# Optimization experiments

Measured on AMD Instinct MI355X. Metric: run time of the kernel, lower is better.

## Reference

```python
import jax, jax.numpy as jnp
import numpy as np

D_MODEL = 1024
NUM_HEADS = 16
D_HEAD = D_MODEL // NUM_HEADS


def setup_inputs() -> dict:
    key = jax.random.key(0)
    ks = jax.random.split(key, 11)
    B, S = 2, 2048
    s = 1.0 / np.sqrt(D_MODEL)
    inp = {
        "Q": jax.random.normal(ks[0], (B, S, D_MODEL), dtype=jnp.float32),
        "K": jax.random.normal(ks[1], (B, S, D_MODEL), dtype=jnp.float32),
        "V": jax.random.normal(ks[2], (B, S, D_MODEL), dtype=jnp.float32),
        "W_q": jax.random.normal(ks[3], (D_MODEL, D_MODEL), dtype=jnp.float32) * s,
        "b_q": jnp.zeros((D_MODEL,), dtype=jnp.float32),
        "W_k": jax.random.normal(ks[4], (D_MODEL, D_MODEL), dtype=jnp.float32) * s,
        "b_k": jnp.zeros((D_MODEL,), dtype=jnp.float32),
        "W_v": jax.random.normal(ks[5], (D_MODEL, D_MODEL), dtype=jnp.float32) * s,
        "b_v": jnp.zeros((D_MODEL,), dtype=jnp.float32),
        "W_o": jax.random.normal(ks[6], (D_MODEL, D_MODEL), dtype=jnp.float32) * s,
        "b_o": jnp.zeros((D_MODEL,), dtype=jnp.float32),
    }
    return inp


def reference(Q, K, V, W_q, b_q, W_k, b_k, W_v, b_v, W_o, b_o):
    B, S, _ = Q.shape
    # Linear projections (torch Linear: x @ W.T + b)
    q = Q @ W_q.T + b_q  # [B,S,D]
    k = K @ W_k.T + b_k
    v = V @ W_v.T + b_v
    # split heads -> [B,H,S,d]
    q = q.reshape(B, S, NUM_HEADS, D_HEAD).transpose(0, 2, 1, 3)
    k = k.reshape(B, S, NUM_HEADS, D_HEAD).transpose(0, 2, 1, 3)
    v = v.reshape(B, S, NUM_HEADS, D_HEAD).transpose(0, 2, 1, 3)
    scores = jnp.einsum("bhqd,bhkd->bhqk", q, k) / np.sqrt(D_HEAD).astype(np.float32)
    attn = jax.nn.softmax(scores, axis=-1)
    out = jnp.einsum("bhqk,bhkd->bhqd", attn, v)
    out = out.transpose(0, 2, 1, 3).reshape(B, S, D_MODEL)
    return out @ W_o.T + b_o
```

## Files before the change

### kernel.cpp

```cpp
#include <hip/hip_runtime.h>
#include <stdint.h>

#define D_MODEL 1024
#define S_LEN   2048
#define BATCH   2
#define NHEAD   16
#define DHEAD   64
#define NTOK    (BATCH * S_LEN)

typedef unsigned short u16;
typedef __attribute__((ext_vector_type(8))) short bf16x8;
typedef __attribute__((ext_vector_type(4))) float f32x4;
typedef __attribute__((ext_vector_type(2))) unsigned int u32x2;

__device__ __forceinline__ unsigned pack2bf(float lo, float hi) {
    unsigned a = __float_as_uint(lo) + 0x8000u;
    unsigned b = __float_as_uint(hi) + 0x8000u;
    return __builtin_amdgcn_perm(b, a, 0x07060302u);
}
__device__ __forceinline__ u16 f2bf1(float f) {
    return (u16)((__float_as_uint(f) + 0x8000u) >> 16);
}

#define GAS(p) ((const __attribute__((address_space(1))) void*)(p))
#define LAS(p) ((__attribute__((address_space(3))) void*)(p))
#define SWZ8(row, c) (((((row) << 3) | ((c) ^ ((row) & 7)))) << 3)

__global__ __launch_bounds__(256) void convert_kernel(
    const float* __restrict__ Q, const float* __restrict__ K, const float* __restrict__ V,
    const float* __restrict__ Wq, const float* __restrict__ Wk,
    const float* __restrict__ Wv, const float* __restrict__ Wo,
    u16* __restrict__ Qb, u16* __restrict__ Kb, u16* __restrict__ Vb,
    u16* __restrict__ Wqb, u16* __restrict__ Wkb, u16* __restrict__ Wvb, u16* __restrict__ Wob)
{
    const size_t SEG = 262144;
    size_t start = (size_t)blockIdx.x * 4096;
    int s = (int)(start / SEG);
    const float* src; u16* dst; size_t seg0;
    if (s < 4)       { src = Q;  dst = Qb;  seg0 = 0; }
    else if (s < 8)  { src = K;  dst = Kb;  seg0 = 4 * SEG; }
    else if (s < 12) { src = V;  dst = Vb;  seg0 = 8 * SEG; }
    else if (s == 12){ src = Wq; dst = Wqb; seg0 = 12 * SEG; }
    else if (s == 13){ src = Wk; dst = Wkb; seg0 = 13 * SEG; }
    else if (s == 14){ src = Wv; dst = Wvb; seg0 = 14 * SEG; }
    else             { src = Wo; dst = Wob; seg0 = 15 * SEG; }
    size_t off = start - seg0 + threadIdx.x;
    const float4* s4 = (const float4*)src;
    #pragma unroll
    for (int k = 0; k < 16; ++k) {
        float4 x = s4[off + (size_t)k * 256];
        u32x2 p = (u32x2){pack2bf(x.x, x.y), pack2bf(x.z, x.w)};
        *(u32x2*)(dst + (off + (size_t)k * 256) * 4) = p;
    }
}

__global__ __launch_bounds__(256) void proj_kernel(
    const u16* __restrict__ Qb, const u16* __restrict__ Kb, const u16* __restrict__ Vb,
    const u16* __restrict__ Wqb, const u16* __restrict__ Wkb, const u16* __restrict__ Wvb,
    const float* __restrict__ bq, const float* __restrict__ bk, const float* __restrict__ bv,
    u16* __restrict__ qw, u16* __restrict__ kw, u16* __restrict__ vtw)
{
    const int z = blockIdx.z;
    const int bx = blockIdx.x;
    const u16* A    = (z == 0) ? Qb  : (z == 1) ? Kb  : Wvb;
    const u16* B    = (z == 0) ? Wqb : (z == 1) ? Wkb : Vb;
    const float* bias = (z == 0) ? bq : (z == 1) ? bk : bv;
    const int mbase = ((z == 2) ? (bx & 7) : (bx >> 3)) * 128;
    const int nbase = ((z == 2) ? (bx >> 3) : (bx & 7)) * 128;

    const int tid = threadIdx.x, lane = tid & 63, wave = tid >> 6;
    const int m16 = lane & 15, quad = lane >> 4;
    const int wm = wave >> 1, wn = wave & 1;

    __shared__ __align__(16) u16 As[128 * 64];
    __shared__ __align__(16) u16 Bs[128 * 64];

    int srow[4], scg[4];
    #pragma unroll
    for (int c = 0; c < 4; ++c) {
        int p = (wave * 4 + c) * 64 + lane;
        srow[c] = p >> 3;
        scg[c]  = (p & 7) ^ (srow[c] & 7);
    }

    f32x4 acc[4][4];
    #pragma unroll
    for (int mt = 0; mt < 4; ++mt)
        #pragma unroll
        for (int nt = 0; nt < 4; ++nt) acc[mt][nt] = (f32x4){0.f, 0.f, 0.f, 0.f};

    for (int kc = 0; kc < D_MODEL; kc += 64) {
        #pragma unroll
        for (int c = 0; c < 4; ++c) {
            __builtin_amdgcn_global_load_lds(
                GAS(A + (size_t)(mbase + srow[c]) * D_MODEL + kc + scg[c] * 8),
                LAS(As + (wave * 4 + c) * 512), 16, 0, 0);
            __builtin_amdgcn_global_load_lds(
                GAS(B + (size_t)(nbase + srow[c]) * D_MODEL + kc + scg[c] * 8),
                LAS(Bs + (wave * 4 + c) * 512), 16, 0, 0);
        }
        __syncthreads();
        #pragma unroll
        for (int half = 0; half < 2; ++half) {
            bf16x8 af[4], bfr[4];
            #pragma unroll
            for (int mt = 0; mt < 4; ++mt)
                af[mt] = *(const bf16x8*)&As[SWZ8(wm * 64 + mt * 16 + m16, quad + 4 * half)];
            #pragma unroll
            for (int nt = 0; nt < 4; ++nt)
                bfr[nt] = *(const bf16x8*)&Bs[SWZ8(wn * 64 + nt * 16 + m16, quad + 4 * half)];
            #pragma unroll
            for (int mt = 0; mt < 4; ++mt)
                #pragma unroll
                for (int nt = 0; nt < 4; ++nt)
                    acc[mt][nt] = __builtin_amdgcn_mfma_f32_16x16x32_bf16(af[mt], bfr[nt], acc[mt][nt], 0, 0, 0);
        }
        __syncthreads();
    }

    if (z < 2) {
        u16* dst = z ? kw : qw;
        const float scale = z ? 1.0f : 0.18033688011112042f;
        #pragma unroll
        for (int nt = 0; nt < 4; ++nt) {
            int gn = nbase + wn * 64 + nt * 16 + m16;
            float bb = bias[gn];
            #pragma unroll
            for (int mt = 0; mt < 4; ++mt)
                #pragma unroll
                for (int r = 0; r < 4; ++r) {
                    int gm = mbase + wm * 64 + mt * 16 + quad * 4 + r;
                    dst[(size_t)gm * D_MODEL + gn] = f2bf1((acc[mt][nt][r] + bb) * scale);
                }
        }
    } else {
        #pragma unroll
        for (int mt = 0; mt < 4; ++mt)
            #pragma unroll
            for (int r = 0; r < 4; ++r) {
                int gm = mbase + wm * 64 + mt * 16 + quad * 4 + r;
                float bb = bias[gm];
                #pragma unroll
                for (int nt = 0; nt < 4; ++nt) {
                    int gn = nbase + wn * 64 + nt * 16 + m16;
                    vtw[(size_t)gm * NTOK + gn] = f2bf1(acc[mt][nt][r] + bb);
                }
            }
    }
}

__global__ __launch_bounds__(256, 4) void attn_kernel(
    const u16* __restrict__ qw, const u16* __restrict__ kw,
    const u16* __restrict__ vtw, u16* __restrict__ aw)
{
    const int qbase = blockIdx.x * 128;
    const int h = blockIdx.y, b = blockIdx.z;
    const int tid = threadIdx.x, lane = tid & 63, wave = tid >> 6;
    const int m16 = lane & 15, quad = lane >> 4;
    const int colbase = h * DHEAD;
    const size_t qrow0 = (size_t)b * S_LEN + qbase;

    __shared__ __align__(16) u16 Ks[2][64 * 64];
    __shared__ __align__(16) u16 Vs[2][64 * 64];
    __shared__ __align__(16) u16 Ps[4][32][72];

    int srow[2], scg[2];
    #pragma unroll
    for (int i = 0; i < 2; ++i) {
        int p = (wave * 2 + i) * 64 + lane;
        srow[i] = p >> 3;
        scg[i]  = (p & 7) ^ (srow[i] & 7);
    }

    #define STAGE_KV(buf, kv0)                                                              \
        do {                                                                                \
            _Pragma("unroll")                                                               \
            for (int i_ = 0; i_ < 2; ++i_) {                                                \
                __builtin_amdgcn_global_load_lds(                                           \
                    GAS(kw + ((size_t)b * S_LEN + (kv0) + srow[i_]) * D_MODEL + colbase + scg[i_] * 8), \
                    LAS(Ks[buf] + (wave * 2 + i_) * 512), 16, 0, 0);                        \
                __builtin_amdgcn_global_load_lds(                                           \
                    GAS(vtw + (size_t)(colbase + srow[i_]) * NTOK + (size_t)b * S_LEN + (kv0) + scg[i_] * 8), \
                    LAS(Vs[buf] + (wave * 2 + i_) * 512), 16, 0, 0);                        \
            }                                                                               \
        } while (0)

    bf16x8 qf[2][2];
    #pragma unroll
    for (int mt = 0; mt < 2; ++mt)
        #pragma unroll
        for (int half = 0; half < 2; ++half)
            qf[mt][half] = *(const bf16x8*)(qw + (qrow0 + wave * 32 + mt * 16 + m16) * D_MODEL
                                            + colbase + quad * 8 + 32 * half);

    STAGE_KV(0, 0);

    float l[2][4];
    f32x4 o[2][4];
    #pragma unroll
    for (int mt = 0; mt < 2; ++mt) {
        #pragma unroll
        for (int r = 0; r < 4; ++r) l[mt][r] = 0.f;
        #pragma unroll
        for (int nt = 0; nt < 4; ++nt) o[mt][nt] = (f32x4){0.f, 0.f, 0.f, 0.f};
    }

    __syncthreads();

    for (int t = 0; t < S_LEN / 64; ++t) {
        const int cur = t & 1;
        if (t + 1 < S_LEN / 64) STAGE_KV(!cur, (t + 1) * 64);

        bf16x8 kf[4][2];
        #pragma unroll
        for (int nt = 0; nt < 4; ++nt)
            #pragma unroll
            for (int half = 0; half < 2; ++half)
                kf[nt][half] = *(const bf16x8*)&Ks[cur][SWZ8(nt * 16 + m16, quad + 4 * half)];

        f32x4 s[2][4];
        #pragma unroll
        for (int mt = 0; mt < 2; ++mt)
            #pragma unroll
            for (int nt = 0; nt < 4; ++nt) {
                s[mt][nt] = (f32x4){-12.f, -12.f, -12.f, -12.f};
                s[mt][nt] = __builtin_amdgcn_mfma_f32_16x16x32_bf16(qf[mt][0], kf[nt][0], s[mt][nt], 0, 0, 0);
                s[mt][nt] = __builtin_amdgcn_mfma_f32_16x16x32_bf16(qf[mt][1], kf[nt][1], s[mt][nt], 0, 0, 0);
            }

        bf16x8 vf[4][2];
        #pragma unroll
        for (int nt = 0; nt < 4; ++nt)
            #pragma unroll
            for (int half = 0; half < 2; ++half)
                vf[nt][half] = *(const bf16x8*)&Vs[cur][SWZ8(nt * 16 + m16, quad + 4 * half)];

        #pragma unroll
        for (int mt = 0; mt < 2; ++mt)
            #pragma unroll
            for (int r = 0; r < 4; ++r) {
                float p0 = __builtin_amdgcn_exp2f(s[mt][0][r]);
                float p1 = __builtin_amdgcn_exp2f(s[mt][1][r]);
                float p2 = __builtin_amdgcn_exp2f(s[mt][2][r]);
                float p3 = __builtin_amdgcn_exp2f(s[mt][3][r]);
                l[mt][r] += (p0 + p1) + (p2 + p3);
                int prow = mt * 16 + quad * 4 + r;
                Ps[wave][prow][0 * 16 + m16] = f2bf1(p0);
                Ps[wave][prow][1 * 16 + m16] = f2bf1(p1);
                Ps[wave][prow][2 * 16 + m16] = f2bf1(p2);
                Ps[wave][prow][3 * 16 + m16] = f2bf1(p3);
            }

        bf16x8 pf[2][2];
        #pragma unroll
        for (int mt = 0; mt < 2; ++mt)
            #pragma unroll
            for (int half = 0; half < 2; ++half)
                pf[mt][half] = *(const bf16x8*)&Ps[wave][mt * 16 + m16][half * 32 + quad * 8];

        #pragma unroll
        for (int mt = 0; mt < 2; ++mt)
            #pragma unroll
            for (int nt = 0; nt < 4; ++nt) {
                o[mt][nt] = __builtin_amdgcn_mfma_f32_16x16x32_bf16(pf[mt][0], vf[nt][0], o[mt][nt], 0, 0, 0);
                o[mt][nt] = __builtin_amdgcn_mfma_f32_16x16x32_bf16(pf[mt][1], vf[nt][1], o[mt][nt], 0, 0, 0);
            }

        __syncthreads();
    }

    #pragma unroll
    for (int mt = 0; mt < 2; ++mt)
        #pragma unroll
        for (int r = 0; r < 4; ++r) {
            float lv = l[mt][r];
            #pragma unroll
            for (int d = 1; d < 16; d <<= 1) lv += __shfl_xor(lv, d, 16);
            float inv = 1.0f / lv;
            size_t gm = qrow0 + wave * 32 + mt * 16 + quad * 4 + r;
            #pragma unroll
            for (int nt = 0; nt < 4; ++nt)
                aw[gm * D_MODEL + colbase + nt * 16 + m16] = f2bf1(o[mt][nt][r] * inv);
        }
    #undef STAGE_KV
}

__global__ __launch_bounds__(256) void outproj_kernel(
    const u16* __restrict__ aw, const u16* __restrict__ Wob,
    const float* __restrict__ bo, float* __restrict__ out)
{
    const int mbase = blockIdx.y * 64;
    const int nbase = blockIdx.x * 128;
    const int tid = threadIdx.x, lane = tid & 63, wave = tid >> 6;
    const int m16 = lane & 15, quad = lane >> 4;

    __shared__ __align__(16) u16 As[64 * 64];
    __shared__ __align__(16) u16 Bs[128 * 64];

    int arow[2], acg[2], brow[4], bcg[4];
    #pragma unroll
    for (int c = 0; c < 2; ++c) {
        int p = (wave * 2 + c) * 64 + lane;
        arow[c] = p >> 3; acg[c] = (p & 7) ^ (arow[c] & 7);
    }
    #pragma unroll
    for (int c = 0; c < 4; ++c) {
        int p = (wave * 4 + c) * 64 + lane;
        brow[c] = p >> 3; bcg[c] = (p & 7) ^ (brow[c] & 7);
    }

    f32x4 acc[4][2];
    #pragma unroll
    for (int mt = 0; mt < 4; ++mt)
        #pragma unroll
        for (int nt = 0; nt < 2; ++nt) acc[mt][nt] = (f32x4){0.f, 0.f, 0.f, 0.f};

    for (int kc = 0; kc < D_MODEL; kc += 64) {
        #pragma unroll
        for (int c = 0; c < 2; ++c)
            __builtin_amdgcn_global_load_lds(
                GAS(aw + (size_t)(mbase + arow[c]) * D_MODEL + kc + acg[c] * 8),
                LAS(As + (wave * 2 + c) * 512), 16, 0, 0);
        #pragma unroll
        for (int c = 0; c < 4; ++c)
            __builtin_amdgcn_global_load_lds(
                GAS(Wob + (size_t)(nbase + brow[c]) * D_MODEL + kc + bcg[c] * 8),
                LAS(Bs + (wave * 4 + c) * 512), 16, 0, 0);
        __syncthreads();
        #pragma unroll
        for (int half = 0; half < 2; ++half) {
            bf16x8 af[4], bfr[2];
            #pragma unroll
            for (int mt = 0; mt < 4; ++mt)
                af[mt] = *(const bf16x8*)&As[SWZ8(mt * 16 + m16, quad + 4 * half)];
            #pragma unroll
            for (int nt = 0; nt < 2; ++nt)
                bfr[nt] = *(const bf16x8*)&Bs[SWZ8(wave * 32 + nt * 16 + m16, quad + 4 * half)];
            #pragma unroll
            for (int mt = 0; mt < 4; ++mt)
                #pragma unroll
                for (int nt = 0; nt < 2; ++nt)
                    acc[mt][nt] = __builtin_amdgcn_mfma_f32_16x16x32_bf16(af[mt], bfr[nt], acc[mt][nt], 0, 0, 0);
        }
        __syncthreads();
    }

    #pragma unroll
    for (int nt = 0; nt < 2; ++nt) {
        int gn = nbase + wave * 32 + nt * 16 + m16;
        float bb = bo[gn];
        #pragma unroll
        for (int mt = 0; mt < 4; ++mt)
            #pragma unroll
            for (int r = 0; r < 4; ++r) {
                int gm = mbase + mt * 16 + quad * 4 + r;
                out[(size_t)gm * D_MODEL + gn] = acc[mt][nt][r] + bb;
            }
    }
}

extern "C" void kernel_launch(void* const* d_in, const int* in_sizes, int n_in,
                              void* d_out, int out_size, void* d_ws, size_t ws_size,
                              hipStream_t stream) {
    const float* Q  = (const float*)d_in[0];
    const float* K  = (const float*)d_in[1];
    const float* V  = (const float*)d_in[2];
    const float* Wq = (const float*)d_in[3];
    const float* bq = (const float*)d_in[4];
    const float* Wk = (const float*)d_in[5];
    const float* bk = (const float*)d_in[6];
    const float* Wv = (const float*)d_in[7];
    const float* bv = (const float*)d_in[8];
    const float* Wo = (const float*)d_in[9];
    const float* bo = (const float*)d_in[10];

    const size_t NT = (size_t)NTOK * D_MODEL;
    const size_t WN = (size_t)D_MODEL * D_MODEL;
    u16* base = (u16*)d_ws;
    u16* qw  = base;
    u16* kw  = base + NT;
    u16* vtw = base + 2 * NT;
    u16* Qb  = base + 3 * NT;
    u16* Kb  = base + 4 * NT;
    u16* Vb  = base + 5 * NT;
    u16* Wqb = base + 6 * NT;
    u16* Wkb = Wqb + WN;
    u16* Wvb = Wkb + WN;
    u16* Wob = Wvb + WN;
    u16* aww = Qb;

    convert_kernel<<<1024, 256, 0, stream>>>(Q, K, V, Wq, Wk, Wv, Wo,
                                             Qb, Kb, Vb, Wqb, Wkb, Wvb, Wob);
    proj_kernel<<<dim3(256, 1, 3), 256, 0, stream>>>(Qb, Kb, Vb, Wqb, Wkb, Wvb,
                                                     bq, bk, bv, qw, kw, vtw);
    attn_kernel<<<dim3(S_LEN / 128, NHEAD, BATCH), 256, 0, stream>>>(qw, kw, vtw, aww);
    outproj_kernel<<<dim3(D_MODEL / 128, NTOK / 64), 256, 0, stream>>>(
        aww, Wob, bo, (float*)d_out);
}
```

Before: 234.9 us.

## Transpose MFMA operand roles to vectorize epilogue stores and shrink attention query tiles

The Q/K projection and output projection now put the weights in the A operand and the tokens in the B operand, so each lane holds four consecutive output features. Those results are written with packed 8-byte bf16 stores or float4 stores instead of scalar 2-byte or 4-byte stores. Attention now computes S^T = K·Q^T with 16 query rows per wave and 64 per block, which doubles the grid. The P tile goes through a swizzled per-wave LDS buffer using packed writes. The aim is to cut uncoalesced stores and LDS traffic, at the cost of less K/V reuse per block, since each block now loads K/V for half as many queries.

```diff
diff --git a/kernel.cpp b/kernel.cpp
--- a/kernel.cpp
+++ b/kernel.cpp
@@ -62,11 +62,11 @@
 {
     const int z = blockIdx.z;
     const int bx = blockIdx.x;
-    const u16* A    = (z == 0) ? Qb  : (z == 1) ? Kb  : Wvb;
-    const u16* B    = (z == 0) ? Wqb : (z == 1) ? Wkb : Vb;
+    const u16* A = (z == 0) ? Wqb : (z == 1) ? Wkb : Wvb;
+    const u16* B = (z == 0) ? Qb  : (z == 1) ? Kb  : Vb;
     const float* bias = (z == 0) ? bq : (z == 1) ? bk : bv;
-    const int mbase = ((z == 2) ? (bx & 7) : (bx >> 3)) * 128;
-    const int nbase = ((z == 2) ? (bx >> 3) : (bx & 7)) * 128;
+    const int mbase = (bx & 7) * 128;
+    const int nbase = (bx >> 3) * 128;
 
     const int tid = threadIdx.x, lane = tid & 63, wave = tid >> 6;
     const int m16 = lane & 15, quad = lane >> 4;
@@ -119,31 +119,34 @@
     }
 
     if (z < 2) {
-        u16* dst = z ? kw : qw;
+        u16* Y = z ? kw : qw;
         const float scale = z ? 1.0f : 0.18033688011112042f;
         #pragma unroll
-        for (int nt = 0; nt < 4; ++nt) {
-            int gn = nbase + wn * 64 + nt * 16 + m16;
-            float bb = bias[gn];
-            #pragma unroll
-            for (int mt = 0; mt < 4; ++mt)
-                #pragma unroll
-                for (int r = 0; r < 4; ++r) {
-                    int gm = mbase + wm * 64 + mt * 16 + quad * 4 + r;
-                    dst[(size_t)gm * D_MODEL + gn] = f2bf1((acc[mt][nt][r] + bb) * scale);
-                }
+        for (int mt = 0; mt < 4; ++mt) {
+            int d0 = mbase + wm * 64 + mt * 16 + quad * 4;
+            float4 b4 = *(const float4*)&bias[d0];
+            #pragma unroll
+            for (int nt = 0; nt < 4; ++nt) {
+                int tok = nbase + wn * 64 + nt * 16 + m16;
+                float v0 = (acc[mt][nt][0] + b4.x) * scale;
+                float v1 = (acc[mt][nt][1] + b4.y) * scale;
+                float v2 = (acc[mt][nt][2] + b4.z) * scale;
+                float v3 = (acc[mt][nt][3] + b4.w) * scale;
+                *(u32x2*)(Y + (size_t)tok * D_MODEL + d0) =
+                    (u32x2){pack2bf(v0, v1), pack2bf(v2, v3)};
+            }
         }
     } else {
         #pragma unroll
         for (int mt = 0; mt < 4; ++mt)
             #pragma unroll
             for (int r = 0; r < 4; ++r) {
-                int gm = mbase + wm * 64 + mt * 16 + quad * 4 + r;
-                float bb = bias[gm];
+                int dout = mbase + wm * 64 + mt * 16 + quad * 4 + r;
+                float bb = bias[dout];
                 #pragma unroll
                 for (int nt = 0; nt < 4; ++nt) {
-                    int gn = nbase + wn * 64 + nt * 16 + m16;
-                    vtw[(size_t)gm * NTOK + gn] = f2bf1(acc[mt][nt][r] + bb);
+                    int tok = nbase + wn * 64 + nt * 16 + m16;
+                    vtw[(size_t)dout * NTOK + tok] = f2bf1(acc[mt][nt][r] + bb);
                 }
             }
     }
@@ -153,7 +156,7 @@
     const u16* __restrict__ qw, const u16* __restrict__ kw,
     const u16* __restrict__ vtw, u16* __restrict__ aw)
 {
-    const int qbase = blockIdx.x * 128;
+    const int qbase = blockIdx.x * 64;
     const int h = blockIdx.y, b = blockIdx.z;
     const int tid = threadIdx.x, lane = tid & 63, wave = tid >> 6;
     const int m16 = lane & 15, quad = lane >> 4;
@@ -162,7 +165,8 @@
 
     __shared__ __align__(16) u16 Ks[2][64 * 64];
     __shared__ __align__(16) u16 Vs[2][64 * 64];
-    __shared__ __align__(16) u16 Ps[4][32][72];
+    __shared__ __align__(16) u16 Pt[4][16 * 64];
+    u16* ptw = Pt[wave];
 
     int srow[2], scg[2];
     #pragma unroll
@@ -185,103 +189,80 @@
             }                                                                               \
         } while (0)
 
-    bf16x8 qf[2][2];
-    #pragma unroll
-    for (int mt = 0; mt < 2; ++mt)
-        #pragma unroll
-        for (int half = 0; half < 2; ++half)
-            qf[mt][half] = *(const bf16x8*)(qw + (qrow0 + wave * 32 + mt * 16 + m16) * D_MODEL
-                                            + colbase + quad * 8 + 32 * half);
+    bf16x8 qf[2];
+    #pragma unroll
+    for (int half = 0; half < 2; ++half)
+        qf[half] = *(const bf16x8*)(qw + (qrow0 + wave * 16 + m16) * D_MODEL
+                                    + colbase + half * 32 + quad * 8);
 
     STAGE_KV(0, 0);
 
-    float l[2][4];
-    f32x4 o[2][4];
-    #pragma unroll
-    for (int mt = 0; mt < 2; ++mt) {
-        #pragma unroll
-        for (int r = 0; r < 4; ++r) l[mt][r] = 0.f;
-        #pragma unroll
-        for (int nt = 0; nt < 4; ++nt) o[mt][nt] = (f32x4){0.f, 0.f, 0.f, 0.f};
-    }
-
+    float l = 0.f;
+    f32x4 o[4];
+    #pragma unroll
+    for (int nt = 0; nt < 4; ++nt) o[nt] = (f32x4){0.f, 0.f, 0.f, 0.f};
+
+    const int M = m16 & 7;
     __syncthreads();
 
     for (int t = 0; t < S_LEN / 64; ++t) {
         const int cur = t & 1;
         if (t + 1 < S_LEN / 64) STAGE_KV(!cur, (t + 1) * 64);
 
-        bf16x8 kf[4][2];
-        #pragma unroll
-        for (int nt = 0; nt < 4; ++nt)
+        f32x4 s[4];
+        #pragma unroll
+        for (int nt = 0; nt < 4; ++nt) {
+            bf16x8 kf0 = *(const bf16x8*)&Ks[cur][SWZ8(nt * 16 + m16, quad)];
+            bf16x8 kf1 = *(const bf16x8*)&Ks[cur][SWZ8(nt * 16 + m16, quad + 4)];
+            s[nt] = (f32x4){-12.f, -12.f, -12.f, -12.f};
+            s[nt] = __builtin_amdgcn_mfma_f32_16x16x32_bf16(kf0, qf[0], s[nt], 0, 0, 0);
+            s[nt] = __builtin_amdgcn_mfma_f32_16x16x32_bf16(kf1, qf[1], s[nt], 0, 0, 0);
+        }
+
+        bf16x8 vf[4][2];
+        #pragma unroll
+        for (int ntd = 0; ntd < 4; ++ntd)
             #pragma unroll
             for (int half = 0; half < 2; ++half)
-                kf[nt][half] = *(const bf16x8*)&Ks[cur][SWZ8(nt * 16 + m16, quad + 4 * half)];
-
-        f32x4 s[2][4];
-        #pragma unroll
-        for (int mt = 0; mt < 2; ++mt)
-            #pragma unroll
-            for (int nt = 0; nt < 4; ++nt) {
-                s[mt][nt] = (f32x4){-12.f, -12.f, -12.f, -12.f};
-                s[mt][nt] = __builtin_amdgcn_mfma_f32_16x16x32_bf16(qf[mt][0], kf[nt][0], s[mt][nt], 0, 0, 0);
-                s[mt][nt] = __builtin_amdgcn_mfma_f32_16x16x32_bf16(qf[mt][1], kf[nt][1], s[mt][nt], 0, 0, 0);
-            }
-
-        bf16x8 vf[4][2];
-        #pragma unroll
-        for (int nt = 0; nt < 4; ++nt)
-            #pragma unroll
-            for (int half = 0; half < 2; ++half)
-                vf[nt][half] = *(const bf16x8*)&Vs[cur][SWZ8(nt * 16 + m16, quad + 4 * half)];
-
-        #pragma unroll
-        for (int mt = 0; mt < 2; ++mt)
-            #pragma unroll
-            for (int r = 0; r < 4; ++r) {
-                float p0 = __builtin_amdgcn_exp2f(s[mt][0][r]);
-                float p1 = __builtin_amdgcn_exp2f(s[mt][1][r]);
-                float p2 = __builtin_amdgcn_exp2f(s[mt][2][r]);
-                float p3 = __builtin_amdgcn_exp2f(s[mt][3][r]);
-                l[mt][r] += (p0 + p1) + (p2 + p3);
-                int prow = mt * 16 + quad * 4 + r;
-                Ps[wave][prow][0 * 16 + m16] = f2bf1(p0);
-                Ps[wave][prow][1 * 16 + m16] = f2bf1(p1);
-                Ps[wave][prow][2 * 16 + m16] = f2bf1(p2);
-                Ps[wave][prow][3 * 16 + m16] = f2bf1(p3);
-            }
-
-        bf16x8 pf[2][2];
-        #pragma unroll
-        for (int mt = 0; mt < 2; ++mt)
-            #pragma unroll
-            for (int half = 0; half < 2; ++half)
-                pf[mt][half] = *(const bf16x8*)&Ps[wave][mt * 16 + m16][half * 32 + quad * 8];
-
-        #pragma unroll
-        for (int mt = 0; mt < 2; ++mt)
-            #pragma unroll
-            for (int nt = 0; nt < 4; ++nt) {
-                o[mt][nt] = __builtin_amdgcn_mfma_f32_16x16x32_bf16(pf[mt][0], vf[nt][0], o[mt][nt], 0, 0, 0);
-                o[mt][nt] = __builtin_amdgcn_mfma_f32_16x16x32_bf16(pf[mt][1], vf[nt][1], o[mt][nt], 0, 0, 0);
-            }
-
-        __syncthreads();
-    }
-
-    #pragma unroll
-    for (int mt = 0; mt < 2; ++mt)
-        #pragma unroll
-        for (int r = 0; r < 4; ++r) {
-            float lv = l[mt][r];
-            #pragma unroll
-            for (int d = 1; d < 16; d <<= 1) lv += __shfl_xor(lv, d, 16);
-            float inv = 1.0f / lv;
-            size_t gm = qrow0 + wave * 32 + mt * 16 + quad * 4 + r;
-            #pragma unroll
-            for (int nt = 0; nt < 4; ++nt)
-                aw[gm * D_MODEL + colbase + nt * 16 + m16] = f2bf1(o[mt][nt][r] * inv);
-        }
+                vf[ntd][half] = *(const bf16x8*)&Vs[cur][SWZ8(ntd * 16 + m16, quad + 4 * half)];
+
+        #pragma unroll
+        for (int nt = 0; nt < 4; ++nt) {
+            float p0 = __builtin_amdgcn_exp2f(s[nt][0]);
+            float p1 = __builtin_amdgcn_exp2f(s[nt][1]);
+            float p2 = __builtin_amdgcn_exp2f(s[nt][2]);
+            float p3 = __builtin_amdgcn_exp2f(s[nt][3]);
+            l += (p0 + p1) + (p2 + p3);
+            int c = nt * 4 + quad;
+            int cs = (((c >> 1) ^ M) << 1) | (c & 1);
+            *(u32x2*)&ptw[m16 * 64 + cs * 4] = (u32x2){pack2bf(p0, p1), pack2bf(p2, p3)};
+        }
+
+        bf16x8 pf[2];
+        #pragma unroll
+        for (int half = 0; half < 2; ++half)
+            pf[half] = *(const bf16x8*)&ptw[m16 * 64 + ((half * 4 + quad) ^ M) * 8];
+
+        #pragma unroll
+        for (int ntd = 0; ntd < 4; ++ntd) {
+            o[ntd] = __builtin_amdgcn_mfma_f32_16x16x32_bf16(vf[ntd][0], pf[0], o[ntd], 0, 0, 0);
+            o[ntd] = __builtin_amdgcn_mfma_f32_16x16x32_bf16(vf[ntd][1], pf[1], o[ntd], 0, 0, 0);
+        }
+
+        __syncthreads();
+    }
+
+    l += __shfl_xor(l, 16);
+    l += __shfl_xor(l, 32);
+    float inv = 1.0f / l;
+
+    size_t orow = (qrow0 + wave * 16 + m16) * D_MODEL + colbase;
+    #pragma unroll
+    for (int ntd = 0; ntd < 4; ++ntd) {
+        float v0 = o[ntd][0] * inv, v1 = o[ntd][1] * inv;
+        float v2 = o[ntd][2] * inv, v3 = o[ntd][3] * inv;
+        *(u32x2*)(aw + orow + ntd * 16 + quad * 4) = (u32x2){pack2bf(v0, v1), pack2bf(v2, v3)};
+    }
     #undef STAGE_KV
 }
 
@@ -289,23 +270,24 @@
     const u16* __restrict__ aw, const u16* __restrict__ Wob,
     const float* __restrict__ bo, float* __restrict__ out)
 {
-    const int mbase = blockIdx.y * 64;
-    const int nbase = blockIdx.x * 128;
+    const int nbase = blockIdx.x * 64;
+    const int mbase = blockIdx.y * 128;
     const int tid = threadIdx.x, lane = tid & 63, wave = tid >> 6;
     const int m16 = lane & 15, quad = lane >> 4;
-
-    __shared__ __align__(16) u16 As[64 * 64];
-    __shared__ __align__(16) u16 Bs[128 * 64];
-
-    int arow[2], acg[2], brow[4], bcg[4];
+    const int wm = wave >> 1, wn = wave & 1;
+
+    __shared__ __align__(16) u16 As[128 * 64];
+    __shared__ __align__(16) u16 Bs[64 * 64];
+
+    int arow[4], acg[4], brow[2], bcg[2];
+    #pragma unroll
+    for (int c = 0; c < 4; ++c) {
+        int p = (wave * 4 + c) * 64 + lane;
+        arow[c] = p >> 3; acg[c] = (p & 7) ^ (arow[c] & 7);
+    }
     #pragma unroll
     for (int c = 0; c < 2; ++c) {
         int p = (wave * 2 + c) * 64 + lane;
-        arow[c] = p >> 3; acg[c] = (p & 7) ^ (arow[c] & 7);
-    }
-    #pragma unroll
-    for (int c = 0; c < 4; ++c) {
-        int p = (wave * 4 + c) * 64 + lane;
         brow[c] = p >> 3; bcg[c] = (p & 7) ^ (brow[c] & 7);
     }
 
@@ -316,26 +298,26 @@
         for (int nt = 0; nt < 2; ++nt) acc[mt][nt] = (f32x4){0.f, 0.f, 0.f, 0.f};
 
     for (int kc = 0; kc < D_MODEL; kc += 64) {
+        #pragma unroll
+        for (int c = 0; c < 4; ++c)
+            __builtin_amdgcn_global_load_lds(
+                GAS(Wob + (size_t)(mbase + arow[c]) * D_MODEL + kc + acg[c] * 8),
+                LAS(As + (wave * 4 + c) * 512), 16, 0, 0);
         #pragma unroll
         for (int c = 0; c < 2; ++c)
             __builtin_amdgcn_global_load_lds(
-                GAS(aw + (size_t)(mbase + arow[c]) * D_MODEL + kc + acg[c] * 8),
-                LAS(As + (wave * 2 + c) * 512), 16, 0, 0);
-        #pragma unroll
-        for (int c = 0; c < 4; ++c)
-            __builtin_amdgcn_global_load_lds(
-                GAS(Wob + (size_t)(nbase + brow[c]) * D_MODEL + kc + bcg[c] * 8),
-                LAS(Bs + (wave * 4 + c) * 512), 16, 0, 0);
+                GAS(aw + (size_t)(nbase + brow[c]) * D_MODEL + kc + bcg[c] * 8),
+                LAS(Bs + (wave * 2 + c) * 512), 16, 0, 0);
         __syncthreads();
         #pragma unroll
         for (int half = 0; half < 2; ++half) {
             bf16x8 af[4], bfr[2];
             #pragma unroll
             for (int mt = 0; mt < 4; ++mt)
-                af[mt] = *(const bf16x8*)&As[SWZ8(mt * 16 + m16, quad + 4 * half)];
+                af[mt] = *(const bf16x8*)&As[SWZ8(wm * 64 + mt * 16 + m16, quad + 4 * half)];
             #pragma unroll
             for (int nt = 0; nt < 2; ++nt)
-                bfr[nt] = *(const bf16x8*)&Bs[SWZ8(wave * 32 + nt * 16 + m16, quad + 4 * half)];
+                bfr[nt] = *(const bf16x8*)&Bs[SWZ8(wn * 32 + nt * 16 + m16, quad + 4 * half)];
             #pragma unroll
             for (int mt = 0; mt < 4; ++mt)
                 #pragma unroll
@@ -346,16 +328,19 @@
     }
 
     #pragma unroll
-    for (int nt = 0; nt < 2; ++nt) {
-        int gn = nbase + wave * 32 + nt * 16 + m16;
-        float bb = bo[gn];
-        #pragma unroll
-        for (int mt = 0; mt < 4; ++mt)
-            #pragma unroll
-            for (int r = 0; r < 4; ++r) {
-                int gm = mbase + mt * 16 + quad * 4 + r;
-                out[(size_t)gm * D_MODEL + gn] = acc[mt][nt][r] + bb;
-            }
+    for (int mt = 0; mt < 4; ++mt) {
+        int d0 = mbase + wm * 64 + mt * 16 + quad * 4;
+        float4 b4 = *(const float4*)&bo[d0];
+        #pragma unroll
+        for (int nt = 0; nt < 2; ++nt) {
+            int tok = nbase + wn * 32 + nt * 16 + m16;
+            float4 st;
+            st.x = acc[mt][nt][0] + b4.x;
+            st.y = acc[mt][nt][1] + b4.y;
+            st.z = acc[mt][nt][2] + b4.z;
+            st.w = acc[mt][nt][3] + b4.w;
+            *(float4*)(out + (size_t)tok * D_MODEL + d0) = st;
+        }
     }
 }
 
@@ -393,7 +378,7 @@
                                              Qb, Kb, Vb, Wqb, Wkb, Wvb, Wob);
     proj_kernel<<<dim3(256, 1, 3), 256, 0, stream>>>(Qb, Kb, Vb, Wqb, Wkb, Wvb,
                                                      bq, bk, bv, qw, kw, vtw);
-    attn_kernel<<<dim3(S_LEN / 128, NHEAD, BATCH), 256, 0, stream>>>(qw, kw, vtw, aww);
-    outproj_kernel<<<dim3(D_MODEL / 128, NTOK / 64), 256, 0, stream>>>(
+    attn_kernel<<<dim3(S_LEN / 64, NHEAD, BATCH), 256, 0, stream>>>(qw, kw, vtw, aww);
+    outproj_kernel<<<dim3(NTOK / 64, D_MODEL / 128), 256, 0, stream>>>(
         aww, Wob, bo, (float*)d_out);
 }
```

Result: slower. 240.9 us (+2.5%).
